# Kernel optimization log

Measured on AMD Instinct MI355X. Metric: run time of the kernel, lower is better.

The kernel has to match this reference:

```python
import jax, jax.numpy as jnp
import numpy as np

B, S, D, H = 4, 2048, 1024, 16
HD = D // H


def setup_inputs() -> dict:
    key = jax.random.key(0)
    kx, kq, kk, kv, ko = jax.random.split(key, 5)
    scale = np.float32(1.0 / np.sqrt(D))
    return {
        "x": jax.random.normal(kx, (B, S, D), dtype=jnp.float32),
        "attention_mask": jnp.ones((B, S), dtype=jnp.int32),
        "Wq": jax.random.normal(kq, (D, D), dtype=jnp.float32) * scale,
        "Wk": jax.random.normal(kk, (D, D), dtype=jnp.float32) * scale,
        "Wv": jax.random.normal(kv, (D, D), dtype=jnp.float32) * scale,
        "Wo": jax.random.normal(ko, (D, D), dtype=jnp.float32) * scale,
    }


def reference(x, attention_mask, Wq, Wk, Wv, Wo):
    b, s, d = x.shape
    h, hd = H, d // H
    # project and split heads: [b, h, s, hd]
    q = (x @ Wq).reshape(b, s, h, hd).transpose(0, 2, 1, 3)
    k = (x @ Wk).reshape(b, s, h, hd).transpose(0, 2, 1, 3)
    v = (x @ Wv).reshape(b, s, h, hd).transpose(0, 2, 1, 3)
    inv_sqrt_hd = np.float32(1.0 / np.sqrt(hd))
    score = jnp.einsum("bhqd,bhkd->bhqk", q, k) * inv_sqrt_hd  # [b,h,s,s]
    idx = jnp.arange(s)
    causal_mask = (idx[None, :] <= idx[:, None])[None, None]  # [1,1,s,s]
    key_mask = attention_mask.astype(bool)[:, None, None, :]  # [b,1,1,s]
    score = jnp.where(causal_mask & key_mask, score, -jnp.inf)
    attn = jax.nn.softmax(score, axis=-1)
    out = jnp.einsum("bhqk,bhkd->bhqd", attn, v)  # [b,h,s,hd]
    out = out.transpose(0, 2, 1, 3).reshape(b, s, d)
    return out @ Wo
```

## Files before the change

kernel.cpp:

```cpp
#include <hip/hip_runtime.h>

typedef __attribute__((ext_vector_type(8))) short short8;
typedef __attribute__((ext_vector_type(4))) float floatx4;
typedef __attribute__((address_space(3))) void lvoid;
typedef const __attribute__((address_space(1))) void gvoid;

#define LOG2E 1.44269504088896340736f

__device__ __forceinline__ ushort f2bf(float f) {
  union { float f; unsigned u; } v; v.f = f;
  unsigned r = v.u + 0x7fffu + ((v.u >> 16) & 1u);
  return (ushort)(r >> 16);
}

__device__ __forceinline__ void gld16(const void* g, void* l) {
  __builtin_amdgcn_global_load_lds((gvoid*)g, (lvoid*)l, 16, 0, 0);
}

__global__ __launch_bounds__(256) void k_prep_x(const float* __restrict__ X,
                                                ushort* __restrict__ Xb) {
  const size_t i = ((size_t)blockIdx.x * 256 + threadIdx.x) * 8;
  float4 v0 = *(const float4*)(X + i);
  float4 v1 = *(const float4*)(X + i + 4);
  ushort u[8] = {f2bf(v0.x), f2bf(v0.y), f2bf(v0.z), f2bf(v0.w),
                 f2bf(v1.x), f2bf(v1.y), f2bf(v1.z), f2bf(v1.w)};
  *(uint4*)(Xb + i) = *(uint4*)u;
}

__global__ __launch_bounds__(256) void k_prep_wt(
    const float* __restrict__ W0, const float* __restrict__ W1,
    const float* __restrict__ W2, const float* __restrict__ W3,
    ushort* __restrict__ T0, ushort* __restrict__ T1,
    ushort* __restrict__ T2, ushort* __restrict__ T3) {
  __shared__ ushort T[64][66];
  const int z = blockIdx.z;
  const float* W = z == 0 ? W0 : (z == 1 ? W1 : (z == 2 ? W2 : W3));
  ushort* Wt = z == 0 ? T0 : (z == 1 ? T1 : (z == 2 ? T2 : T3));
  const int kb = blockIdx.x * 64, nb = blockIdx.y * 64;
  const int t = threadIdx.x, r = t >> 2, c0 = (t & 3) * 16;
  const float* src = W + (size_t)(kb + r) * 1024 + nb + c0;
  #pragma unroll
  for (int i = 0; i < 4; i++) {
    float4 a = ((const float4*)src)[i];
    T[r][c0 + i*4 + 0] = f2bf(a.x); T[r][c0 + i*4 + 1] = f2bf(a.y);
    T[r][c0 + i*4 + 2] = f2bf(a.z); T[r][c0 + i*4 + 3] = f2bf(a.w);
  }
  __syncthreads();
  ushort u[16];
  #pragma unroll
  for (int j = 0; j < 16; j++) u[j] = T[c0 + j][r];
  ushort* dst = Wt + (size_t)(nb + r) * 1024 + kb + c0;
  ((uint4*)dst)[0] = ((uint4*)u)[0];
  ((uint4*)dst)[1] = ((uint4*)u)[1];
}

#define GEMM_LOOP(Aptr, BTptr, BFptr)                                          \
  constexpr int LDB = PREPPED ? 32 : 40;                                       \
  __shared__ __align__(16) ushort As[128 * 32];                                \
  __shared__ __align__(16) ushort Bs[128 * LDB];                               \
  const int tid = threadIdx.x, l = tid & 63, w = tid >> 6;                     \
  const int wm = w >> 1, wn = w & 1, lr = l & 15, lk = l >> 4;                 \
  const int m0 = blockIdx.y * 128, n0 = blockIdx.x * 128;                      \
  const int srow = l >> 2;                                                     \
  const int scol = ((l & 3) ^ ((l >> 3) & 3)) * 8;                             \
  const int c0 = w * 2;                                                        \
  const int xchunk = (lk ^ ((lr >> 1) & 3)) * 8;                               \
  const int bk = tid >> 3, bn = (tid & 7) * 16;                                \
  floatx4 acc[4][4] = {};                                                      \
  for (int kt = 0; kt < 1024; kt += 32) {                                      \
    __syncthreads();                                                           \
    _Pragma("unroll")                                                          \
    for (int i = 0; i < 2; i++) {                                              \
      const int c = c0 + i;                                                    \
      gld16(Aptr + (size_t)(m0 + c*16 + srow) * 1024 + kt + scol, &As[c*512]); \
      if constexpr (PREPPED)                                                   \
        gld16(BTptr + (size_t)(n0 + c*16 + srow) * 1024 + kt + scol,           \
              &Bs[c*512]);                                                     \
    }                                                                          \
    if constexpr (!PREPPED) {                                                  \
      const float* src = BFptr + (size_t)(kt + bk) * 1024 + n0 + bn;           \
      float vb[16];                                                            \
      _Pragma("unroll")                                                        \
      for (int i = 0; i < 4; i++) ((float4*)vb)[i] = ((const float4*)src)[i];  \
      _Pragma("unroll")                                                        \
      for (int i = 0; i < 16; i++) Bs[(bn + i) * 40 + bk] = f2bf(vb[i]);       \
    }                                                                          \
    __syncthreads();                                                           \
    short8 af[4], bfr[4];                                                      \
    _Pragma("unroll")                                                          \
    for (int f = 0; f < 4; f++) {                                              \
      af[f] = *(const short8*)&As[(wm*64 + f*16 + lr) * 32 + xchunk];          \
      if constexpr (PREPPED)                                                   \
        bfr[f] = *(const short8*)&Bs[(wn*64 + f*16 + lr) * 32 + xchunk];       \
      else                                                                     \
        bfr[f] = *(const short8*)&Bs[(wn*64 + f*16 + lr) * 40 + lk*8];         \
    }                                                                          \
    _Pragma("unroll")                                                          \
    for (int i = 0; i < 4; i++)                                                \
      _Pragma("unroll")                                                        \
      for (int j = 0; j < 4; j++)                                              \
        acc[i][j] = __builtin_amdgcn_mfma_f32_16x16x32_bf16(af[i], bfr[j],     \
                                                            acc[i][j], 0,0,0);\
  }

template <bool PREPPED>
__global__ __launch_bounds__(256) void k_proj(
    const ushort* __restrict__ Xb,
    const ushort* __restrict__ Wtq, const ushort* __restrict__ Wtk,
    const ushort* __restrict__ Wtv,
    const float* __restrict__ Wfq, const float* __restrict__ Wfk,
    const float* __restrict__ Wfv,
    ushort* __restrict__ Qo, ushort* __restrict__ Ko, ushort* __restrict__ Vo)
{
  const int z = blockIdx.z;
  const ushort* Bt = PREPPED ? (z == 0 ? Wtq : (z == 1 ? Wtk : Wtv)) : nullptr;
  const float*  Bf = PREPPED ? nullptr : (z == 0 ? Wfq : (z == 1 ? Wfk : Wfv));
  ushort* Out = z == 0 ? Qo : (z == 1 ? Ko : Vo);
  const float scale = z == 0 ? 0.125f : 1.0f;
  GEMM_LOOP(Xb, Bt, Bf)
  if (z == 2) {
    #pragma unroll
    for (int i = 0; i < 4; i++) {
      const int m = m0 + wm*64 + i*16 + lk*4;
      const int bb = m >> 11, s = m & 2047;
      #pragma unroll
      for (int j = 0; j < 4; j++) {
        const int n = n0 + wn*64 + j*16 + lr;
        const int h = n >> 6, hd = n & 63;
        ushort u4[4];
        #pragma unroll
        for (int r = 0; r < 4; r++) u4[r] = f2bf(acc[i][j][r]);
        *(uint2*)(Out + (((size_t)(bb*16 + h)) * 64 + hd) * 2048 + s) = *(uint2*)u4;
      }
    }
  } else {
    #pragma unroll
    for (int i = 0; i < 4; i++) {
      #pragma unroll
      for (int j = 0; j < 4; j++) {
        const int n = n0 + wn*64 + j*16 + lr;
        const int h = n >> 6, hd = n & 63;
        #pragma unroll
        for (int r = 0; r < 4; r++) {
          const int m = m0 + wm*64 + i*16 + lk*4 + r;
          const int bb = m >> 11, s = m & 2047;
          Out[(((size_t)(bb*16 + h)) * 2048 + s) * 64 + hd] = f2bf(acc[i][j][r] * scale);
        }
      }
    }
  }
}

template <bool PREPPED>
__global__ __launch_bounds__(256) void k_out(
    const ushort* __restrict__ A, const ushort* __restrict__ Wt,
    const float* __restrict__ Wf, float* __restrict__ Out)
{
  GEMM_LOOP(A, Wt, Wf)
  #pragma unroll
  for (int i = 0; i < 4; i++) {
    #pragma unroll
    for (int j = 0; j < 4; j++) {
      const int n = n0 + wn*64 + j*16 + lr;
      #pragma unroll
      for (int r = 0; r < 4; r++) {
        const int m = m0 + wm*64 + i*16 + lk*4 + r;
        Out[(size_t)m * 1024 + n] = acc[i][j][r];
      }
    }
  }
}

__global__ __launch_bounds__(256) void k_attn(
    const ushort* __restrict__ Q, const ushort* __restrict__ K,
    const ushort* __restrict__ V, const int* __restrict__ amask,
    ushort* __restrict__ AO)
{
  __shared__ __align__(16) ushort Kl[64 * 64];
  __shared__ __align__(16) ushort Vl[64 * 64];
  __shared__ __align__(16) ushort Pl[4][16 * 72];

  const int tid = threadIdx.x, l = tid & 63, w = tid >> 6;
  const int lr = l & 15, lk = l >> 4;
  const int g = blockIdx.x;
  const int swz = (g & 7) * 128 + (g >> 3);
  const int p = swz & 15, bh = swz >> 4;
  const int b = bh >> 4, h = bh & 15;
  const int qA0 = p * 64, qB0 = (31 - p) * 64;

  const ushort* Qbh = Q + (size_t)bh * 2048 * 64;
  const ushort* Kbh = K + (size_t)bh * 2048 * 64;
  const ushort* Vbh = V + (size_t)bh * 64 * 2048;

  const int qrA = qA0 + w*16 + lr, qrB = qB0 + w*16 + lr;
  short8 aqA0 = *(const short8*)(Qbh + (size_t)qrA * 64 + lk*8);
  short8 aqA1 = *(const short8*)(Qbh + (size_t)qrA * 64 + 32 + lk*8);
  short8 aqB0 = *(const short8*)(Qbh + (size_t)qrB * 64 + lk*8);
  short8 aqB1 = *(const short8*)(Qbh + (size_t)qrB * 64 + 32 + lk*8);

  floatx4 oA[4] = {}, oB[4] = {};
  float mmA = -1e30f, llA = 0.f, mmB = -1e30f, llB = 0.f;

  const int krow = l >> 3;
  const int kcol = ((l & 7) ^ krow) * 8;

  const int kend = 31 - p;
  const int amb = b * 2048;
  int kv0 = 0;

  auto process = [&](const short8& q0f, const short8& q1f, floatx4* o,
                     float& mm, float& ll, int qbase, bool diag,
                     float mval, bool allv) {
    floatx4 sa[4] = {};
    #pragma unroll
    for (int f = 0; f < 4; f++) {
      const int rb = f*16 + lr;
      const int cs = (rb & 7) * 8;
      short8 k0 = *(const short8*)&Kl[rb*64 + ((lk*8) ^ cs)];
      short8 k1 = *(const short8*)&Kl[rb*64 + (((4+lk)*8) ^ cs)];
      sa[f] = __builtin_amdgcn_mfma_f32_16x16x32_bf16(k0, q0f, sa[f], 0,0,0);
      sa[f] = __builtin_amdgcn_mfma_f32_16x16x32_bf16(k1, q1f, sa[f], 0,0,0);
    }
    if (!allv) {
      #pragma unroll
      for (int f = 0; f < 4; f++)
        #pragma unroll
        for (int r = 0; r < 4; r++)
          sa[f][r] += __shfl(mval, f*16 + lk*4 + r, 64);
    }
    if (diag) {
      const int q = qbase + w*16 + lr;
      #pragma unroll
      for (int f = 0; f < 4; f++)
        #pragma unroll
        for (int r = 0; r < 4; r++)
          if (kv0 + f*16 + lk*4 + r > q) sa[f][r] = -1e30f;
    }
    float mx = sa[0][0];
    #pragma unroll
    for (int f = 0; f < 4; f++)
      #pragma unroll
      for (int r = 0; r < 4; r++) mx = fmaxf(mx, sa[f][r]);
    mx = fmaxf(mx, __shfl_xor(mx, 16, 64));
    mx = fmaxf(mx, __shfl_xor(mx, 32, 64));
    if (!__all(mx <= mm + 8.f)) {
      const float pm = fmaxf(mm, mx);
      const float scl = __builtin_exp2f((mm - pm) * LOG2E);
      mm = pm;
      ll *= scl;
      float sclo[4];
      #pragma unroll
      for (int r = 0; r < 4; r++) sclo[r] = __shfl(scl, lk*4 + r, 64);
      #pragma unroll
      for (int f = 0; f < 4; f++)
        #pragma unroll
        for (int r = 0; r < 4; r++) o[f][r] *= sclo[r];
    }
    const float nm = mm * LOG2E;
    float rs = 0.f;
    #pragma unroll
    for (int f = 0; f < 4; f++)
      #pragma unroll
      for (int r = 0; r < 4; r++) {
        float pv = __builtin_exp2f(__builtin_fmaf(sa[f][r], LOG2E, -nm));
        sa[f][r] = pv;
        rs += pv;
      }
    rs += __shfl_xor(rs, 16, 64);
    rs += __shfl_xor(rs, 32, 64);
    ll += rs;
    #pragma unroll
    for (int f = 0; f < 4; f++) {
      unsigned pk0, pk1;
      asm("v_cvt_pk_bf16_f32 %0, %1, %2" : "=v"(pk0)
          : "v"(sa[f][0]), "v"(sa[f][1]));
      asm("v_cvt_pk_bf16_f32 %0, %1, %2" : "=v"(pk1)
          : "v"(sa[f][2]), "v"(sa[f][3]));
      *(uint2*)&Pl[w][lr*72 + f*16 + lk*4] = make_uint2(pk0, pk1);
    }
    asm volatile("s_waitcnt lgkmcnt(0)" ::: "memory");
    __builtin_amdgcn_sched_barrier(0);
    short8 ap0 = *(const short8*)&Pl[w][lr*72 + lk*8];
    short8 ap1 = *(const short8*)&Pl[w][lr*72 + 32 + lk*8];
    #pragma unroll
    for (int f = 0; f < 4; f++) {
      const int rb = f*16 + lr;
      const int cs = (rb & 7) * 8;
      short8 bv0 = *(const short8*)&Vl[rb*64 + ((lk*8) ^ cs)];
      short8 bv1 = *(const short8*)&Vl[rb*64 + (((4+lk)*8) ^ cs)];
      o[f] = __builtin_amdgcn_mfma_f32_16x16x32_bf16(ap0, bv0, o[f], 0,0,0);
      o[f] = __builtin_amdgcn_mfma_f32_16x16x32_bf16(ap1, bv1, o[f], 0,0,0);
    }
  };

  for (int t = 0; t <= kend; t++) {
    kv0 = t * 64;
    const int am = amask[amb + kv0 + l];
    const bool allv = __all(am != 0);
    const float mval = am ? 0.f : -1e30f;
    __syncthreads();
    #pragma unroll
    for (int i = 0; i < 2; i++) {
      const int c = w*2 + i;
      gld16(Kbh + (size_t)(kv0 + c*8 + krow) * 64 + kcol, &Kl[c*512]);
      gld16(Vbh + (size_t)(c*8 + krow) * 2048 + kv0 + kcol, &Vl[c*512]);
    }
    __syncthreads();
    process(aqB0, aqB1, oB, mmB, llB, qB0, t == kend, mval, allv);
    if (t <= p) process(aqA0, aqA1, oA, mmA, llA, qA0, t == p, mval, allv);
  }

  const float invA = llA > 0.f ? 1.0f / llA : 0.f;
  const float invB = llB > 0.f ? 1.0f / llB : 0.f;
  float ivA[4], ivB[4];
  #pragma unroll
  for (int r = 0; r < 4; r++) {
    ivA[r] = __shfl(invA, lk*4 + r, 64);
    ivB[r] = __shfl(invB, lk*4 + r, 64);
  }
  #pragma unroll
  for (int r = 0; r < 4; r++) {
    const int sA = qA0 + w*16 + lk*4 + r;
    const int sB = qB0 + w*16 + lk*4 + r;
    const size_t baseA = ((size_t)b * 2048 + sA) * 1024 + h * 64;
    const size_t baseB = ((size_t)b * 2048 + sB) * 1024 + h * 64;
    #pragma unroll
    for (int f = 0; f < 4; f++) {
      AO[baseA + f*16 + lr] = f2bf(oA[f][r] * ivA[r]);
      AO[baseB + f*16 + lr] = f2bf(oB[f][r] * ivB[r]);
    }
  }
}

extern "C" void kernel_launch(void* const* d_in, const int* in_sizes, int n_in,
                              void* d_out, int out_size, void* d_ws, size_t ws_size,
                              hipStream_t stream) {
  const float* x     = (const float*)d_in[0];
  const int*   amask = (const int*)d_in[1];
  const float* Wq    = (const float*)d_in[2];
  const float* Wk    = (const float*)d_in[3];
  const float* Wv    = (const float*)d_in[4];
  const float* Wo    = (const float*)d_in[5];
  float* out = (float*)d_out;

  const size_t NEL = (size_t)4 * 2048 * 1024;
  const size_t WEL = (size_t)1024 * 1024;

  dim3 blk(256);
  const bool prepped = ws_size >= (size_t)76 * 1024 * 1024;

  if (prepped) {
    ushort* Xb  = (ushort*)d_ws;
    ushort* Wtq = Xb + NEL;
    ushort* Wtk = Wtq + WEL;
    ushort* Wtv = Wtk + WEL;
    ushort* Wto = Wtv + WEL;
    ushort* Qb  = Wto + WEL;
    ushort* Kb  = Qb + NEL;
    ushort* Vb  = Kb + NEL;
    ushort* AO  = Xb;

    k_prep_x<<<4096, blk, 0, stream>>>(x, Xb);
    k_prep_wt<<<dim3(16, 16, 4), blk, 0, stream>>>(Wq, Wk, Wv, Wo,
                                                   Wtq, Wtk, Wtv, Wto);
    k_proj<true><<<dim3(8, 64, 3), blk, 0, stream>>>(
        Xb, Wtq, Wtk, Wtv, nullptr, nullptr, nullptr, Qb, Kb, Vb);
    k_attn<<<dim3(1024), blk, 0, stream>>>(Qb, Kb, Vb, amask, AO);
    k_out<true><<<dim3(8, 64), blk, 0, stream>>>(AO, Wto, nullptr, out);
  } else {
    ushort* Xb = (ushort*)d_ws;
    ushort* Qb = Xb + NEL;
    ushort* Kb = Qb + NEL;
    ushort* Vb = Kb + NEL;
    ushort* AO = Xb;

    k_prep_x<<<4096, blk, 0, stream>>>(x, Xb);
    k_proj<false><<<dim3(8, 64, 3), blk, 0, stream>>>(
        Xb, nullptr, nullptr, nullptr, Wq, Wk, Wv, Qb, Kb, Vb);
    k_attn<<<dim3(1024), blk, 0, stream>>>(Qb, Kb, Vb, amask, AO);
    k_out<false><<<dim3(8, 64), blk, 0, stream>>>(AO, nullptr, Wo, out);
  }
}
```

Before: 309.9 us.

## Double-buffer LDS tiles in GEMM and attention, swizzle P buffer, add setprio

Both the projection GEMM loop and the attention KV loop now use two LDS buffers. The next tile's global-to-LDS loads are issued before computing on the current tile, so each iteration needs only one barrier instead of two and load latency can overlap with MFMA work. The attention P scratch buffer drops its row padding in favour of an XOR swizzle to avoid bank conflicts. s_setprio is raised around the MFMA blocks. The cost is doubled LDS use, which may lower occupancy. There is also a possible ordering risk, because the async LDS loads are never explicitly waited on before the current buffer is read.

New measurement: 296.8 us. 1.04x faster.

```diff
diff --git a/kernel.cpp b/kernel.cpp
--- a/kernel.cpp
+++ b/kernel.cpp
@@ -56,8 +56,8 @@
 
 #define GEMM_LOOP(Aptr, BTptr, BFptr)                                          \
   constexpr int LDB = PREPPED ? 32 : 40;                                       \
-  __shared__ __align__(16) ushort As[128 * 32];                                \
-  __shared__ __align__(16) ushort Bs[128 * LDB];                               \
+  __shared__ __align__(16) ushort As[2][128 * 32];                             \
+  __shared__ __align__(16) ushort Bs[2][128 * LDB];                            \
   const int tid = threadIdx.x, l = tid & 63, w = tid >> 6;                     \
   const int wm = w >> 1, wn = w & 1, lr = l & 15, lk = l >> 4;                 \
   const int m0 = blockIdx.y * 128, n0 = blockIdx.x * 128;                      \
@@ -67,40 +67,67 @@
   const int xchunk = (lk ^ ((lr >> 1) & 3)) * 8;                               \
   const int bk = tid >> 3, bn = (tid & 7) * 16;                                \
   floatx4 acc[4][4] = {};                                                      \
+                                       \
+  _Pragma("unroll")                                                            \
+  for (int i = 0; i < 2; i++) {                                                \
+    const int c = c0 + i;                                                      \
+    gld16(Aptr + (size_t)(m0 + c*16 + srow) * 1024 + scol, &As[0][c*512]);     \
+    if constexpr (PREPPED)                                                     \
+      gld16(BTptr + (size_t)(n0 + c*16 + srow) * 1024 + scol, &Bs[0][c*512]);  \
+  }                                                                            \
+  if constexpr (!PREPPED) {                                                    \
+    const float* src = BFptr + (size_t)bk * 1024 + n0 + bn;                    \
+    float vb[16];                                                              \
+    _Pragma("unroll")                                                          \
+    for (int i = 0; i < 4; i++) ((float4*)vb)[i] = ((const float4*)src)[i];    \
+    _Pragma("unroll")                                                          \
+    for (int i = 0; i < 16; i++) Bs[0][(bn + i) * 40 + bk] = f2bf(vb[i]);      \
+  }                                                                            \
   for (int kt = 0; kt < 1024; kt += 32) {                                      \
-    __syncthreads();                                                           \
-    _Pragma("unroll")                                                          \
-    for (int i = 0; i < 2; i++) {                                              \
-      const int c = c0 + i;                                                    \
-      gld16(Aptr + (size_t)(m0 + c*16 + srow) * 1024 + kt + scol, &As[c*512]); \
-      if constexpr (PREPPED)                                                   \
-        gld16(BTptr + (size_t)(n0 + c*16 + srow) * 1024 + kt + scol,           \
-              &Bs[c*512]);                                                     \
+    const int cur = (kt >> 5) & 1, nxt = cur ^ 1;                              \
+    __syncthreads();   \
+    float vbn[16];                                                             \
+    if (kt + 32 < 1024) {                                                      \
+      _Pragma("unroll")                                                        \
+      for (int i = 0; i < 2; i++) {                                            \
+        const int c = c0 + i;                                                  \
+        gld16(Aptr + (size_t)(m0 + c*16 + srow) * 1024 + kt + 32 + scol,       \
+              &As[nxt][c*512]);                                                \
+        if constexpr (PREPPED)                                                 \
+          gld16(BTptr + (size_t)(n0 + c*16 + srow) * 1024 + kt + 32 + scol,    \
+                &Bs[nxt][c*512]);                                              \
+      }                                                                        \
+      if constexpr (!PREPPED) {                                                \
+        const float* src = BFptr + (size_t)(kt + 32 + bk) * 1024 + n0 + bn;    \
+        _Pragma("unroll")                                                      \
+        for (int i = 0; i < 4; i++)                                            \
+          ((float4*)vbn)[i] = ((const float4*)src)[i];                         \
+      }                                                                        \
     }                                                                          \
-    if constexpr (!PREPPED) {                                                  \
-      const float* src = BFptr + (size_t)(kt + bk) * 1024 + n0 + bn;           \
-      float vb[16];                                                            \
-      _Pragma("unroll")                                                        \
-      for (int i = 0; i < 4; i++) ((float4*)vb)[i] = ((const float4*)src)[i];  \
-      _Pragma("unroll")                                                        \
-      for (int i = 0; i < 16; i++) Bs[(bn + i) * 40 + bk] = f2bf(vb[i]);       \
-    }                                                                          \
-    __syncthreads();                                                           \
     short8 af[4], bfr[4];                                                      \
     _Pragma("unroll")                                                          \
     for (int f = 0; f < 4; f++) {                                              \
-      af[f] = *(const short8*)&As[(wm*64 + f*16 + lr) * 32 + xchunk];          \
+      af[f] = *(const short8*)&As[cur][(wm*64 + f*16 + lr) * 32 + xchunk];     \
       if constexpr (PREPPED)                                                   \
-        bfr[f] = *(const short8*)&Bs[(wn*64 + f*16 + lr) * 32 + xchunk];       \
+        bfr[f] = *(const short8*)&Bs[cur][(wn*64 + f*16 + lr) * 32 + xchunk];  \
       else                                                                     \
-        bfr[f] = *(const short8*)&Bs[(wn*64 + f*16 + lr) * 40 + lk*8];         \
+        bfr[f] = *(const short8*)&Bs[cur][(wn*64 + f*16 + lr) * 40 + lk*8];    \
     }                                                                          \
+    __builtin_amdgcn_s_setprio(1);                                             \
     _Pragma("unroll")                                                          \
     for (int i = 0; i < 4; i++)                                                \
       _Pragma("unroll")                                                        \
       for (int j = 0; j < 4; j++)                                              \
         acc[i][j] = __builtin_amdgcn_mfma_f32_16x16x32_bf16(af[i], bfr[j],     \
                                                             acc[i][j], 0,0,0);\
+    __builtin_amdgcn_s_setprio(0);                                             \
+    if constexpr (!PREPPED) {                                                  \
+      if (kt + 32 < 1024) {        \
+        _Pragma("unroll")                                                      \
+        for (int i = 0; i < 16; i++)                                           \
+          Bs[nxt][(bn + i) * 40 + bk] = f2bf(vbn[i]);                          \
+      }                                                                        \
+    }                                                                          \
   }
 
 template <bool PREPPED>
@@ -176,9 +203,9 @@
     const ushort* __restrict__ V, const int* __restrict__ amask,
     ushort* __restrict__ AO)
 {
-  __shared__ __align__(16) ushort Kl[64 * 64];
-  __shared__ __align__(16) ushort Vl[64 * 64];
-  __shared__ __align__(16) ushort Pl[4][16 * 72];
+  __shared__ __align__(16) ushort Kl[2][64 * 64];
+  __shared__ __align__(16) ushort Vl[2][64 * 64];
+  __shared__ __align__(16) ushort Pl[4][16 * 64];
 
   const int tid = threadIdx.x, l = tid & 63, w = tid >> 6;
   const int lr = l & 15, lk = l >> 4;
@@ -208,19 +235,30 @@
   const int amb = b * 2048;
   int kv0 = 0;
 
+  auto stage = [&](int bi, int kv) {
+    #pragma unroll
+    for (int i = 0; i < 2; i++) {
+      const int c = w*2 + i;
+      gld16(Kbh + (size_t)(kv + c*8 + krow) * 64 + kcol, &Kl[bi][c*512]);
+      gld16(Vbh + (size_t)(c*8 + krow) * 2048 + kv + kcol, &Vl[bi][c*512]);
+    }
+  };
+
   auto process = [&](const short8& q0f, const short8& q1f, floatx4* o,
                      float& mm, float& ll, int qbase, bool diag,
-                     float mval, bool allv) {
+                     float mval, bool allv, int cur) {
     floatx4 sa[4] = {};
+    __builtin_amdgcn_s_setprio(1);
     #pragma unroll
     for (int f = 0; f < 4; f++) {
       const int rb = f*16 + lr;
       const int cs = (rb & 7) * 8;
-      short8 k0 = *(const short8*)&Kl[rb*64 + ((lk*8) ^ cs)];
-      short8 k1 = *(const short8*)&Kl[rb*64 + (((4+lk)*8) ^ cs)];
+      short8 k0 = *(const short8*)&Kl[cur][rb*64 + ((lk*8) ^ cs)];
+      short8 k1 = *(const short8*)&Kl[cur][rb*64 + (((4+lk)*8) ^ cs)];
       sa[f] = __builtin_amdgcn_mfma_f32_16x16x32_bf16(k0, q0f, sa[f], 0,0,0);
       sa[f] = __builtin_amdgcn_mfma_f32_16x16x32_bf16(k1, q1f, sa[f], 0,0,0);
     }
+    __builtin_amdgcn_s_setprio(0);
     if (!allv) {
       #pragma unroll
       for (int f = 0; f < 4; f++)
@@ -276,38 +314,37 @@
           : "v"(sa[f][0]), "v"(sa[f][1]));
       asm("v_cvt_pk_bf16_f32 %0, %1, %2" : "=v"(pk1)
           : "v"(sa[f][2]), "v"(sa[f][3]));
-      *(uint2*)&Pl[w][lr*72 + f*16 + lk*4] = make_uint2(pk0, pk1);
+      const int ch = (f*2 + (lk>>1)) ^ (lr & 7);
+      *(uint2*)&Pl[w][lr*64 + ch*8 + (lk&1)*4] = make_uint2(pk0, pk1);
     }
     asm volatile("s_waitcnt lgkmcnt(0)" ::: "memory");
     __builtin_amdgcn_sched_barrier(0);
-    short8 ap0 = *(const short8*)&Pl[w][lr*72 + lk*8];
-    short8 ap1 = *(const short8*)&Pl[w][lr*72 + 32 + lk*8];
+    short8 ap0 = *(const short8*)&Pl[w][lr*64 + ((lk ^ (lr&7)) * 8)];
+    short8 ap1 = *(const short8*)&Pl[w][lr*64 + (((4+lk) ^ (lr&7)) * 8)];
+    __builtin_amdgcn_s_setprio(1);
     #pragma unroll
     for (int f = 0; f < 4; f++) {
       const int rb = f*16 + lr;
       const int cs = (rb & 7) * 8;
-      short8 bv0 = *(const short8*)&Vl[rb*64 + ((lk*8) ^ cs)];
-      short8 bv1 = *(const short8*)&Vl[rb*64 + (((4+lk)*8) ^ cs)];
+      short8 bv0 = *(const short8*)&Vl[cur][rb*64 + ((lk*8) ^ cs)];
+      short8 bv1 = *(const short8*)&Vl[cur][rb*64 + (((4+lk)*8) ^ cs)];
       o[f] = __builtin_amdgcn_mfma_f32_16x16x32_bf16(ap0, bv0, o[f], 0,0,0);
       o[f] = __builtin_amdgcn_mfma_f32_16x16x32_bf16(ap1, bv1, o[f], 0,0,0);
     }
+    __builtin_amdgcn_s_setprio(0);
   };
 
+  stage(0, 0);
   for (int t = 0; t <= kend; t++) {
     kv0 = t * 64;
     const int am = amask[amb + kv0 + l];
+    __syncthreads();
+    if (t < kend) stage((t + 1) & 1, kv0 + 64);
     const bool allv = __all(am != 0);
     const float mval = am ? 0.f : -1e30f;
-    __syncthreads();
-    #pragma unroll
-    for (int i = 0; i < 2; i++) {
-      const int c = w*2 + i;
-      gld16(Kbh + (size_t)(kv0 + c*8 + krow) * 64 + kcol, &Kl[c*512]);
-      gld16(Vbh + (size_t)(c*8 + krow) * 2048 + kv0 + kcol, &Vl[c*512]);
-    }
-    __syncthreads();
-    process(aqB0, aqB1, oB, mmB, llB, qB0, t == kend, mval, allv);
-    if (t <= p) process(aqA0, aqA1, oA, mmA, llA, qA0, t == p, mval, allv);
+    const int cur = t & 1;
+    process(aqB0, aqB1, oB, mmB, llB, qB0, t == kend, mval, allv, cur);
+    if (t <= p) process(aqA0, aqA1, oA, mmA, llA, qA0, t == p, mval, allv, cur);
   }
 
   const float invA = llA > 0.f ? 1.0f / llA : 0.f;
```
